# Optimization experiments

Hardware: AMD Instinct MI355X
Metric: run time of the kernel (lower is better)

The kernel has to match this reference:

```python
import jax, jax.numpy as jnp
import numpy as np

B, T, C, H = 2, 2048, 1024, 16
HD = C // H          # head_dim = 64
HALF = HD // 2       # rope half dim = 32
ROPE_BASE = 10000.0


def _build_sin_cos(seq_len, half_dim, base=ROPE_BASE):
    # mirrors build_sin_cos: angles[t, i] = t * base^(-2i / (2*half_dim))
    pos = jnp.arange(seq_len, dtype=jnp.float32)[:, None]                     # [T,1]
    inv_freq = 1.0 / (base ** (jnp.arange(0, half_dim * 2, 2, dtype=jnp.float32) / (half_dim * 2)))
    angles = pos * inv_freq                                                   # [T, half]
    return jnp.sin(angles), jnp.cos(angles)


def setup_inputs() -> dict:
    key = jax.random.key(0)
    k1, k2, k3 = jax.random.split(key, 3)
    x = jax.random.normal(k1, (B, T, C), dtype=jnp.float32)
    # nn.Linear weights (stored as [out,in] in torch; we keep [in,out] for x @ W)
    Wqkv = jax.random.normal(k2, (C, 3 * C), dtype=jnp.float32) * (C ** -0.5)
    Wproj = jax.random.normal(k3, (C, C), dtype=jnp.float32) * (C ** -0.5)
    rope_sin, rope_cos = _build_sin_cos(T, HALF)
    return {"x": x, "Wqkv": Wqkv, "Wproj": Wproj, "rope_sin": rope_sin, "rope_cos": rope_cos}


def reference(x, Wqkv, Wproj, rope_sin, rope_cos):
    Bb, Tt, Cc = x.shape
    Hh = H
    hd = Cc // Hh
    # fused QKV projection, then per-head split (matches view(B,T,H,3*hd).split)
    qkv = (x @ Wqkv).reshape(Bb, Tt, Hh, 3 * hd)
    q, k, v = jnp.split(qkv, 3, axis=-1)                                      # each [B,T,H,hd]
    # RoPE (single device path: local slice == full range)
    s = rope_sin[:Tt][None, :, None, :].astype(x.dtype)                       # [1,T,1,half]
    c = rope_cos[:Tt][None, :, None, :].astype(x.dtype)

    def rot(t):
        t1, t2 = jnp.split(t, 2, axis=-1)
        return jnp.concatenate([t1 * c - t2 * s, t1 * s + t2 * c], axis=-1)

    q = rot(q)
    k = rot(k)
    # causal scaled dot-product attention (flash_attn default scale = hd^-0.5)
    scale = jnp.asarray(hd, x.dtype) ** -0.5
    scores = jnp.einsum('bqhd,bkhd->bhqk', q, k) * scale                      # [B,H,T,T]
    causal = jnp.tril(jnp.ones((Tt, Tt), dtype=bool))
    scores = jnp.where(causal, scores, jnp.finfo(x.dtype).min)
    probs = jax.nn.softmax(scores, axis=-1)
    attn = jnp.einsum('bhqk,bkhd->bqhd', probs, v).reshape(Bb, Tt, Cc)
    return attn @ Wproj
```

## Files before the change

### kernel.cpp

```cpp
#include <hip/hip_runtime.h>

#define Bb 2
#define Tt 2048
#define Cc_ 1024
#define Hh 16
#define HDd 64

typedef __attribute__((ext_vector_type(8))) short bf16x8;
typedef __attribute__((ext_vector_type(4))) float f32x4;
typedef __attribute__((ext_vector_type(4))) unsigned short u16x4;
typedef __attribute__((ext_vector_type(2))) unsigned int u32x2;

__device__ __forceinline__ unsigned short f2bf(float f) {
  union { float f; unsigned int u; } v; v.f = f;
  unsigned int r = v.u + 0x7FFFu + ((v.u >> 16) & 1u);
  return (unsigned short)(r >> 16);
}
__device__ __forceinline__ float bf2f(unsigned short u) {
  union { unsigned int u; float f; } v; v.u = ((unsigned int)u) << 16;
  return v.f;
}
__device__ __forceinline__ unsigned int cvtpk(float lo, float hi) {
  unsigned int r;
  asm("v_cvt_pk_bf16_f32 %0, %1, %2" : "=v"(r) : "v"(lo), "v"(hi));
  return r;
}
__device__ __forceinline__ f32x4 mfma16(bf16x8 a, bf16x8 b, f32x4 c) {
  return __builtin_amdgcn_mfma_f32_16x16x32_bf16(a, b, c, 0, 0, 0);
}
__device__ __forceinline__ void gl_lds16(const void* g, void* l) {
  auto* gp = reinterpret_cast<const __attribute__((address_space(1))) unsigned int*>(
      reinterpret_cast<unsigned long long>(g));
  auto* lp = reinterpret_cast<__attribute__((address_space(3))) unsigned int*>(
      reinterpret_cast<unsigned long long>(l));
  __builtin_amdgcn_global_load_lds(gp, lp, 16, 0, 0);
}

__global__ __launch_bounds__(256) void k_prep(const float* __restrict__ x,
                                              const float* __restrict__ Wqkv,
                                              const float* __restrict__ Wproj,
                                              unsigned short* __restrict__ xb,
                                              unsigned short* __restrict__ wqkvt,
                                              unsigned short* __restrict__ wprot) {
  const int bid = blockIdx.x;
  const int tid = threadIdx.x;
  if (bid < 4096) {
    const int i = bid * 256 + tid;
    f32x4 v = ((const f32x4*)x)[i];
    u16x4 o;
    o[0] = f2bf(v[0]); o[1] = f2bf(v[1]); o[2] = f2bf(v[2]); o[3] = f2bf(v[3]);
    ((u16x4*)xb)[i] = o;
    return;
  }
  __shared__ float tile[32][33];
  const int tx = tid & 31, ty = tid >> 5;
  if (bid < 4096 + 3072) {
    const int tt = bid - 4096;
    const int n0 = (tt % 96) * 32, k0 = (tt / 96) * 32;
    const int region = n0 >> 10, nl = n0 & 1023;
    const int ob = (nl >> 6) * 192 + region * 64 + (nl & 63);
#pragma unroll
    for (int i = 0; i < 4; ++i)
      tile[ty + i * 8][tx] = Wqkv[(size_t)(k0 + ty + i * 8) * 3072 + ob + tx];
    __syncthreads();
#pragma unroll
    for (int i = 0; i < 4; ++i)
      wqkvt[(size_t)(n0 + ty + i * 8) * 1024 + k0 + tx] = f2bf(tile[tx][ty + i * 8]);
    return;
  }
  const int tt = bid - 7168;
  const int c0 = (tt & 31) * 32, r0 = (tt >> 5) * 32;
#pragma unroll
  for (int i = 0; i < 4; ++i)
    tile[ty + i * 8][tx] = Wproj[(size_t)(r0 + ty + i * 8) * 1024 + c0 + tx];
  __syncthreads();
#pragma unroll
  for (int i = 0; i < 4; ++i)
    wprot[(size_t)(c0 + ty + i * 8) * 1024 + r0 + tx] = f2bf(tile[tx][ty + i * 8]);
}

__global__ __launch_bounds__(256) void k_gemm_qkv(const unsigned short* __restrict__ A,
                                                  const unsigned short* __restrict__ Bt,
                                                  const float* __restrict__ rsin,
                                                  const float* __restrict__ rcos,
                                                  unsigned short* __restrict__ Qo,
                                                  unsigned short* __restrict__ Ko,
                                                  unsigned short* __restrict__ vtmp) {
  __shared__ unsigned short lA[128 * 64];
  __shared__ unsigned short lB[128 * 64];
  const int K = 1024;
  const int tid = threadIdx.x;
  const int lane = tid & 63, wid = tid >> 6;
  const int wr = wid >> 1, wc = wid & 1;
  const int bm = blockIdx.y * 128, bn = blockIdx.x * 128;
  const int l15 = lane & 15, l4 = lane >> 4;
  f32x4 acc[4][4];
#pragma unroll
  for (int i = 0; i < 4; ++i)
#pragma unroll
    for (int j = 0; j < 4; ++j) acc[i][j] = f32x4{0.f, 0.f, 0.f, 0.f};
  for (int t = 0; t < 16; ++t) {
    const int k0 = t << 6;
    __syncthreads();
#pragma unroll
    for (int i = 0; i < 4; ++i) {
      const int slot = i * 256 + tid;
      const int row = slot >> 3, g = slot & 7;
      const int gs = (g ^ (row & 7)) * 8;
      gl_lds16(A + (size_t)(bm + row) * K + k0 + gs, &lA[slot * 8]);
      gl_lds16(Bt + (size_t)(bn + row) * K + k0 + gs, &lB[slot * 8]);
    }
    __syncthreads();
#pragma unroll
    for (int ks = 0; ks < 2; ++ks) {
      bf16x8 af[4], bfr[4];
#pragma unroll
      for (int mf = 0; mf < 4; ++mf) {
        const int row = wr * 64 + mf * 16 + l15;
        const int g = ks * 4 + l4;
        af[mf] = *(const bf16x8*)&lA[row * 64 + ((g ^ (row & 7)) * 8)];
      }
#pragma unroll
      for (int nf = 0; nf < 4; ++nf) {
        const int row = wc * 64 + nf * 16 + l15;
        const int g = ks * 4 + l4;
        bfr[nf] = *(const bf16x8*)&lB[row * 64 + ((g ^ (row & 7)) * 8)];
      }
#pragma unroll
      for (int mf = 0; mf < 4; ++mf)
#pragma unroll
        for (int nf = 0; nf < 4; ++nf)
          acc[mf][nf] = mfma16(af[mf], bfr[nf], acc[mf][nf]);
    }
  }
  const int rb = bm + wr * 64 + l4 * 4;
  const int region = blockIdx.x >> 3;
  if (region < 2) {
    const int h = (blockIdx.x & 7) * 2 + wc;
    unsigned short* dst = (region == 0) ? Qo : Ko;
    const float qs = (region == 0) ? (0.125f * 1.44269504088896f) : 1.0f;
#pragma unroll
    for (int mf = 0; mf < 4; ++mf)
#pragma unroll
      for (int j = 0; j < 4; ++j) {
        const int trow = rb + mf * 16 + j;
        const int bi = trow >> 11, t = trow & 2047;
        const size_t rowb = ((size_t)(bi * Hh + h) * Tt + t) * 64;
#pragma unroll
        for (int nf = 0; nf < 2; ++nf) {
          const int d = nf * 16 + l15;
          const float sn = rsin[t * 32 + d], cs = rcos[t * 32 + d];
          const float a1 = acc[mf][nf][j], a2 = acc[mf][nf + 2][j];
          dst[rowb + d] = f2bf((a1 * cs - a2 * sn) * qs);
          dst[rowb + d + 32] = f2bf((a1 * sn + a2 * cs) * qs);
        }
      }
  } else {
    const int colb = (blockIdx.x & 7) * 128 + wc * 64;
#pragma unroll
    for (int mf = 0; mf < 4; ++mf)
#pragma unroll
      for (int nf = 0; nf < 4; ++nf)
#pragma unroll
        for (int j = 0; j < 4; ++j)
          vtmp[(size_t)(rb + mf * 16 + j) * 1024 + colb + nf * 16 + l15] =
              f2bf(acc[mf][nf][j]);
  }
}

__global__ __launch_bounds__(256) void k_vrep(const unsigned short* __restrict__ vtmp,
                                              unsigned short* __restrict__ Vt) {
  __shared__ unsigned short tile[32][72];
  const int bh = blockIdx.y;
  const int t0 = blockIdx.x * 32;
  const int tx = threadIdx.x, ty = threadIdx.y;
  const int b = bh >> 4, h = bh & 15;
#pragma unroll
  for (int i = 0; i < 4; ++i) {
    const int trow = ty + i * 8;
    const size_t r = (size_t)(b * Tt + t0 + trow) * 1024 + h * 64;
    tile[trow][tx] = vtmp[r + tx];
    tile[trow][tx + 32] = vtmp[r + 32 + tx];
  }
  __syncthreads();
#pragma unroll
  for (int i = 0; i < 8; ++i) {
    const int d = ty + i * 8;
    Vt[((size_t)bh * 64 + d) * Tt + t0 + tx] = tile[tx][d];
  }
}

__global__ __launch_bounds__(256, 4) void k_attn(const unsigned short* __restrict__ Q,
                                                 const unsigned short* __restrict__ Kt,
                                                 const unsigned short* __restrict__ Vt,
                                                 unsigned short* __restrict__ Aout) {
  __shared__ unsigned short lK[2 * 64 * 64];
  __shared__ unsigned short lV[2 * 64 * 64];
  __shared__ unsigned short lP[4 * 16 * 64];
  const int bid = blockIdx.x;
  const int xcd = bid & 7, ss = bid >> 3;
  const int cc = ss & 31, kk = ss >> 5;
  const int bh = xcd * 4 + kk;
  const int c2 = (cc + ((kk & 2) ? 16 : 0)) & 31;
  const int qt = (kk & 1) ? (31 - c2) : c2;
  const int b = bh >> 4, h = bh & 15;
  const int tid = threadIdx.x, lane = tid & 63, w = tid >> 6;
  const int l15 = lane & 15, l4 = lane >> 4;
  const int qb = qt * 64;
  const unsigned short* Kbh = Kt + (size_t)bh * Tt * 64;
  const unsigned short* Vbh = Vt + (size_t)bh * 64 * Tt;

  int fo[4][2];
#pragma unroll
  for (int a = 0; a < 4; ++a)
#pragma unroll
    for (int bb = 0; bb < 2; ++bb)
      fo[a][bb] = ((a * 16 + l15) * 64 + (((bb * 4 + l4) ^ (l15 & 7)) * 8)) * 2;
  int pwo[4];
#pragma unroll
  for (int nf = 0; nf < 4; ++nf)
    pwo[nf] = (l15 * 64 + (((nf * 2 + (l4 >> 1)) ^ (l15 & 7)) * 8) + (l4 & 1) * 4) * 2;
  char* const pB = (char*)lP + w * 2048;
  char* const kB0 = (char*)lK;
  char* const vB0 = (char*)lV;
  const int rA = tid >> 3;
  const int gsA = ((tid & 7) ^ (rA & 7)) * 8;
  const int kgA = rA * 64 + gsA;
  const int vgA = rA * 2048 + gsA;
  char* const ldKA = (char*)lK + tid * 16;
  char* const ldVA = (char*)lV + tid * 16;

#define STAGE(BUF, TT)                                                   \
  {                                                                      \
    const int kv_ = (TT) * 64;                                           \
    gl_lds16(Kbh + kv_ * 64 + kgA, ldKA + (BUF) * 8192);                 \
    gl_lds16(Kbh + kv_ * 64 + kgA + 32 * 64, ldKA + (BUF) * 8192 + 4096);\
    gl_lds16(Vbh + kv_ + vgA, ldVA + (BUF) * 8192);                      \
    gl_lds16(Vbh + kv_ + vgA + 32 * 2048, ldVA + (BUF) * 8192 + 4096);   \
  }

  const size_t qoff = ((size_t)bh * Tt + qb + w * 16 + l15) * 64 + l4 * 8;
  const bf16x8 qf0 = *(const bf16x8*)&Q[qoff];
  const bf16x8 qf1 = *(const bf16x8*)&Q[qoff + 32];
  f32x4 o[4];
#pragma unroll
  for (int i = 0; i < 4; ++i) o[i] = f32x4{0.f, 0.f, 0.f, 0.f};
  float mrun = -1e30f, lrun = 0.f;
  const int nt = qt + 1;

#define BODY(CUR, T, LASTT)                                                       \
  {                                                                               \
    if ((T) + 1 < nt) STAGE(CUR ^ 1, (T) + 1);                                    \
    f32x4 sv[4];                                                                  \
    _Pragma("unroll") for (int i = 0; i < 4; ++i) sv[i] = f32x4{0.f, 0.f, 0.f, 0.f}; \
    __builtin_amdgcn_s_setprio(1);                                                \
    _Pragma("unroll") for (int ks = 0; ks < 2; ++ks) {                            \
      const bf16x8 qa = ks ? qf1 : qf0;                                           \
      _Pragma("unroll") for (int nf = 0; nf < 4; ++nf) {                          \
        const bf16x8 kf = *(const bf16x8*)(kB0 + (CUR) * 8192 + fo[nf][ks]);      \
        sv[nf] = mfma16(kf, qa, sv[nf]);                                          \
      }                                                                           \
    }                                                                             \
    __builtin_amdgcn_s_setprio(0);                                                \
    if (LASTT) {                                                                  \
      _Pragma("unroll") for (int nf = 0; nf < 4; ++nf)                            \
        _Pragma("unroll") for (int j = 0; j < 4; ++j)                             \
          if (nf * 16 + l4 * 4 + j > w * 16 + l15) sv[nf][j] = -3e38f;            \
    }                                                                             \
    float mx = fmaxf(fmaxf(fmaxf(sv[0][0], sv[0][1]), fmaxf(sv[0][2], sv[0][3])), \
                     fmaxf(fmaxf(sv[1][0], sv[1][1]), fmaxf(sv[1][2], sv[1][3])));\
    mx = fmaxf(mx, fmaxf(fmaxf(fmaxf(sv[2][0], sv[2][1]), fmaxf(sv[2][2], sv[2][3])), \
                         fmaxf(fmaxf(sv[3][0], sv[3][1]), fmaxf(sv[3][2], sv[3][3])))); \
    if (!__all(mx - mrun <= 8.0f)) {                                              \
      mx = fmaxf(mx, __shfl_xor(mx, 16, 64));                                     \
      mx = fmaxf(mx, __shfl_xor(mx, 32, 64));                                     \
      const float mnew = fmaxf(mrun, mx);                                         \
      const float alpha = exp2f(mrun - mnew);                                     \
      lrun *= alpha;                                                              \
      float aj[4];                                                                \
      _Pragma("unroll") for (int j = 0; j < 4; ++j) aj[j] = __shfl(alpha, l4 * 4 + j, 64); \
      _Pragma("unroll") for (int df = 0; df < 4; ++df)                            \
        _Pragma("unroll") for (int j = 0; j < 4; ++j) o[df][j] *= aj[j];          \
      mrun = mnew;                                                                \
    }                                                                             \
    _Pragma("unroll") for (int nf = 0; nf < 4; ++nf) {                            \
      const float p0 = exp2f(sv[nf][0] - mrun), p1 = exp2f(sv[nf][1] - mrun);     \
      const float p2 = exp2f(sv[nf][2] - mrun), p3 = exp2f(sv[nf][3] - mrun);     \
      lrun += (p0 + p1) + (p2 + p3);                                              \
      u32x2 pk; pk[0] = cvtpk(p0, p1); pk[1] = cvtpk(p2, p3);                     \
      *(u32x2*)(pB + pwo[nf]) = pk;                                               \
    }                                                                             \
    __builtin_amdgcn_s_setprio(1);                                                \
    _Pragma("unroll") for (int kb = 0; kb < 2; ++kb) {                            \
      const bf16x8 pa = *(const bf16x8*)(pB + fo[0][kb]);                         \
      _Pragma("unroll") for (int df = 0; df < 4; ++df) {                          \
        const bf16x8 vb = *(const bf16x8*)(vB0 + (CUR) * 8192 + fo[df][kb]);      \
        o[df] = mfma16(pa, vb, o[df]);                                            \
      }                                                                           \
    }                                                                             \
    __builtin_amdgcn_s_setprio(0);                                                \
    if ((T) + 1 < nt) asm volatile("s_waitcnt vmcnt(0)" ::: "memory");            \
    __builtin_amdgcn_s_barrier();                                                 \
  }

  STAGE(0, 0);
  asm volatile("s_waitcnt vmcnt(0)" ::: "memory");
  __builtin_amdgcn_s_barrier();
  int t = 0;
  for (; t + 2 < nt; t += 2) {
    BODY(0, t, false);
    BODY(1, t + 1, false);
  }
  if (nt - t == 2) {
    BODY(0, t, false);
    BODY(1, t + 1, true);
  } else {
    BODY(0, t, true);
  }
#undef BODY
#undef STAGE

  lrun += __shfl_xor(lrun, 16, 64);
  lrun += __shfl_xor(lrun, 32, 64);
  const float rinv = 1.f / lrun;
  float lj[4];
#pragma unroll
  for (int j = 0; j < 4; ++j) lj[j] = __shfl(rinv, l4 * 4 + j, 64);
#pragma unroll
  for (int j = 0; j < 4; ++j) {
    const size_t rr = (size_t)(b * Tt + qb + w * 16 + l4 * 4 + j) * 1024 + h * 64 + l15;
#pragma unroll
    for (int df = 0; df < 4; ++df) Aout[rr + df * 16] = f2bf(o[df][j] * lj[j]);
  }
}

__global__ __launch_bounds__(256) void k_gemm2(const unsigned short* __restrict__ A,
                                               const unsigned short* __restrict__ Bt,
                                               float* __restrict__ Cout) {
  __shared__ unsigned short lA[2][128 * 64];
  __shared__ unsigned short lB[2][64 * 64];
  const int K = 1024, N = 1024;
  const int tid = threadIdx.x;
  const int lane = tid & 63, w = tid >> 6;
  const int bm = blockIdx.y * 128, bn = blockIdx.x * 64;
  const int l15 = lane & 15, l4 = lane >> 4;
  f32x4 acc[2][4];
#pragma unroll
  for (int i = 0; i < 2; ++i)
#pragma unroll
    for (int j = 0; j < 4; ++j) acc[i][j] = f32x4{0.f, 0.f, 0.f, 0.f};

#define STG(BUF, TT)                                                        \
  {                                                                         \
    const int k0 = (TT) << 6;                                               \
    _Pragma("unroll") for (int i = 0; i < 4; ++i) {                         \
      const int slot = i * 256 + tid;                                       \
      const int row = slot >> 3, g = slot & 7;                              \
      const int gs = (g ^ (row & 7)) * 8;                                   \
      gl_lds16(A + (size_t)(bm + row) * K + k0 + gs, &lA[BUF][slot * 8]);   \
    }                                                                       \
    _Pragma("unroll") for (int i = 0; i < 2; ++i) {                         \
      const int slot = i * 256 + tid;                                       \
      const int row = slot >> 3, g = slot & 7;                              \
      const int gs = (g ^ (row & 7)) * 8;                                   \
      gl_lds16(Bt + (size_t)(bn + row) * K + k0 + gs, &lB[BUF][slot * 8]);  \
    }                                                                       \
  }

  STG(0, 0);
  asm volatile("s_waitcnt vmcnt(0)" ::: "memory");
  __builtin_amdgcn_s_barrier();
  for (int t = 0; t < 16; ++t) {
    const int cur = t & 1;
    if (t + 1 < 16) STG(cur ^ 1, t + 1);
    __builtin_amdgcn_s_setprio(1);
#pragma unroll
    for (int ks = 0; ks < 2; ++ks) {
      bf16x8 af[2], bfr[4];
#pragma unroll
      for (int mf = 0; mf < 2; ++mf) {
        const int row = w * 32 + mf * 16 + l15;
        const int g = ks * 4 + l4;
        af[mf] = *(const bf16x8*)&lA[cur][row * 64 + ((g ^ (row & 7)) * 8)];
      }
#pragma unroll
      for (int nf = 0; nf < 4; ++nf) {
        const int row = nf * 16 + l15;
        const int g = ks * 4 + l4;
        bfr[nf] = *(const bf16x8*)&lB[cur][row * 64 + ((g ^ (row & 7)) * 8)];
      }
#pragma unroll
      for (int mf = 0; mf < 2; ++mf)
#pragma unroll
        for (int nf = 0; nf < 4; ++nf)
          acc[mf][nf] = mfma16(af[mf], bfr[nf], acc[mf][nf]);
    }
    __builtin_amdgcn_s_setprio(0);
    if (t + 1 < 16) asm volatile("s_waitcnt vmcnt(0)" ::: "memory");
    __builtin_amdgcn_s_barrier();
  }
#undef STG
  const int rb = bm + w * 32 + l4 * 4;
  const int cb = bn + l15;
#pragma unroll
  for (int mf = 0; mf < 2; ++mf)
#pragma unroll
    for (int nf = 0; nf < 4; ++nf)
#pragma unroll
      for (int j = 0; j < 4; ++j)
        Cout[(size_t)(rb + mf * 16 + j) * N + cb + nf * 16] = acc[mf][nf][j];
}

extern "C" void kernel_launch(void* const* d_in, const int* in_sizes, int n_in,
                              void* d_out, int out_size, void* d_ws, size_t ws_size,
                              hipStream_t stream) {
  const float* x = (const float*)d_in[0];
  const float* Wqkv = (const float*)d_in[1];
  const float* Wproj = (const float*)d_in[2];
  const float* rsin = (const float*)d_in[3];
  const float* rcos = (const float*)d_in[4];
  float* out = (float*)d_out;
  char* ws = (char*)d_ws;
  unsigned short* xb = (unsigned short*)(ws);
  unsigned short* wqkvt = (unsigned short*)(ws + (size_t)(8 << 20));
  unsigned short* wprot = (unsigned short*)(ws + (size_t)(14 << 20));
  unsigned short* vtmp = (unsigned short*)(ws + (size_t)(16 << 20));
  unsigned short* Q = (unsigned short*)(ws + (size_t)(40 << 20));
  unsigned short* K = (unsigned short*)(ws + (size_t)(48 << 20));
  unsigned short* Vt = (unsigned short*)(ws + (size_t)(56 << 20));
  unsigned short* attn = (unsigned short*)(ws + (size_t)(64 << 20));

  k_prep<<<8192, 256, 0, stream>>>(x, Wqkv, Wproj, xb, wqkvt, wprot);
  k_gemm_qkv<<<dim3(24, 32), 256, 0, stream>>>(xb, wqkvt, rsin, rcos, Q, K, vtmp);
  k_vrep<<<dim3(64, 32), dim3(32, 8), 0, stream>>>(vtmp, Vt);
  k_attn<<<1024, 256, 0, stream>>>(Q, K, Vt, attn);
  k_gemm2<<<dim3(16, 32), 256, 0, stream>>>(attn, wprot, out);
}
```

Before: 186.3 us.

## Double-buffer QKV GEMM loads and fuse V transpose into its epilogue

The QKV GEMM now double-buffers its LDS tiles. The next K-slice's global-to-LDS copy is issued before the MFMAs on the current slice, with one barrier per iteration and raised wave priority during compute. The V region's epilogue transposes the tile through LDS and writes Vt directly, which removes the separate k_vrep kernel and the vtmp round trip through global memory. In exchange, LDS use doubles to 64KB per block, which may lower occupancy, and the epilogue adds two extra barrier phases.

```diff
diff --git a/kernel.cpp b/kernel.cpp
--- a/kernel.cpp
+++ b/kernel.cpp
@@ -85,9 +85,9 @@
                                                   const float* __restrict__ rcos,
                                                   unsigned short* __restrict__ Qo,
                                                   unsigned short* __restrict__ Ko,
-                                                  unsigned short* __restrict__ vtmp) {
-  __shared__ unsigned short lA[128 * 64];
-  __shared__ unsigned short lB[128 * 64];
+                                                  unsigned short* __restrict__ Vt) {
+  __shared__ unsigned short lA[2][128 * 64];
+  __shared__ unsigned short lB[2][128 * 64];
   const int K = 1024;
   const int tid = threadIdx.x;
   const int lane = tid & 63, wid = tid >> 6;
@@ -99,18 +99,26 @@
   for (int i = 0; i < 4; ++i)
 #pragma unroll
     for (int j = 0; j < 4; ++j) acc[i][j] = f32x4{0.f, 0.f, 0.f, 0.f};
+
+#define STG(BUF, TT)                                                        \
+  {                                                                         \
+    const int k0 = (TT) << 6;                                               \
+    _Pragma("unroll") for (int i = 0; i < 4; ++i) {                         \
+      const int slot = i * 256 + tid;                                       \
+      const int row = slot >> 3, g = slot & 7;                              \
+      const int gs = (g ^ (row & 7)) * 8;                                   \
+      gl_lds16(A + (size_t)(bm + row) * K + k0 + gs, &lA[BUF][slot * 8]);   \
+      gl_lds16(Bt + (size_t)(bn + row) * K + k0 + gs, &lB[BUF][slot * 8]);  \
+    }                                                                       \
+  }
+
+  STG(0, 0);
+  asm volatile("s_waitcnt vmcnt(0)" ::: "memory");
+  __builtin_amdgcn_s_barrier();
   for (int t = 0; t < 16; ++t) {
-    const int k0 = t << 6;
-    __syncthreads();
-#pragma unroll
-    for (int i = 0; i < 4; ++i) {
-      const int slot = i * 256 + tid;
-      const int row = slot >> 3, g = slot & 7;
-      const int gs = (g ^ (row & 7)) * 8;
-      gl_lds16(A + (size_t)(bm + row) * K + k0 + gs, &lA[slot * 8]);
-      gl_lds16(Bt + (size_t)(bn + row) * K + k0 + gs, &lB[slot * 8]);
-    }
-    __syncthreads();
+    const int cur = t & 1;
+    if (t + 1 < 16) STG(cur ^ 1, t + 1);
+    __builtin_amdgcn_s_setprio(1);
 #pragma unroll
     for (int ks = 0; ks < 2; ++ks) {
       bf16x8 af[4], bfr[4];
@@ -118,13 +126,13 @@
       for (int mf = 0; mf < 4; ++mf) {
         const int row = wr * 64 + mf * 16 + l15;
         const int g = ks * 4 + l4;
-        af[mf] = *(const bf16x8*)&lA[row * 64 + ((g ^ (row & 7)) * 8)];
+        af[mf] = *(const bf16x8*)&lA[cur][row * 64 + ((g ^ (row & 7)) * 8)];
       }
 #pragma unroll
       for (int nf = 0; nf < 4; ++nf) {
         const int row = wc * 64 + nf * 16 + l15;
         const int g = ks * 4 + l4;
-        bfr[nf] = *(const bf16x8*)&lB[row * 64 + ((g ^ (row & 7)) * 8)];
+        bfr[nf] = *(const bf16x8*)&lB[cur][row * 64 + ((g ^ (row & 7)) * 8)];
       }
 #pragma unroll
       for (int mf = 0; mf < 4; ++mf)
@@ -132,7 +140,12 @@
         for (int nf = 0; nf < 4; ++nf)
           acc[mf][nf] = mfma16(af[mf], bfr[nf], acc[mf][nf]);
     }
-  }
+    __builtin_amdgcn_s_setprio(0);
+    if (t + 1 < 16) asm volatile("s_waitcnt vmcnt(0)" ::: "memory");
+    __builtin_amdgcn_s_barrier();
+  }
+#undef STG
+
   const int rb = bm + wr * 64 + l4 * 4;
   const int region = blockIdx.x >> 3;
   if (region < 2) {
@@ -156,37 +169,35 @@
         }
       }
   } else {
-    const int colb = (blockIdx.x & 7) * 128 + wc * 64;
-#pragma unroll
-    for (int mf = 0; mf < 4; ++mf)
-#pragma unroll
-      for (int nf = 0; nf < 4; ++nf)
-#pragma unroll
-        for (int j = 0; j < 4; ++j)
-          vtmp[(size_t)(rb + mf * 16 + j) * 1024 + colb + nf * 16 + l15] =
-              f2bf(acc[mf][nf][j]);
-  }
-}
-
-__global__ __launch_bounds__(256) void k_vrep(const unsigned short* __restrict__ vtmp,
-                                              unsigned short* __restrict__ Vt) {
-  __shared__ unsigned short tile[32][72];
-  const int bh = blockIdx.y;
-  const int t0 = blockIdx.x * 32;
-  const int tx = threadIdx.x, ty = threadIdx.y;
-  const int b = bh >> 4, h = bh & 15;
-#pragma unroll
-  for (int i = 0; i < 4; ++i) {
-    const int trow = ty + i * 8;
-    const size_t r = (size_t)(b * Tt + t0 + trow) * 1024 + h * 64;
-    tile[trow][tx] = vtmp[r + tx];
-    tile[trow][tx + 32] = vtmp[r + 32 + tx];
-  }
-  __syncthreads();
-#pragma unroll
-  for (int i = 0; i < 8; ++i) {
-    const int d = ty + i * 8;
-    Vt[((size_t)bh * 64 + d) * Tt + t0 + tx] = tile[tx][d];
+    unsigned short* tp = &lA[0][0];
+    const int h0 = (blockIdx.x & 7) * 2;
+    const int bi = bm >> 11, tbase = bm & 2047;
+    const int dd = tid >> 2, t0c = (tid & 3) * 32;
+#pragma unroll
+    for (int ph = 0; ph < 2; ++ph) {
+      if (wc == ph) {
+#pragma unroll
+        for (int mf = 0; mf < 4; ++mf)
+#pragma unroll
+          for (int nf = 0; nf < 4; ++nf)
+#pragma unroll
+            for (int j = 0; j < 4; ++j) {
+              const int tl = wr * 64 + mf * 16 + l4 * 4 + j;
+              const int dl = nf * 16 + l15;
+              tp[tl * 65 + dl] = f2bf(acc[mf][nf][j]);
+            }
+      }
+      __syncthreads();
+      const size_t ob = ((size_t)(bi * Hh + h0 + ph) * 64 + dd) * (size_t)Tt + tbase + t0c;
+#pragma unroll
+      for (int c = 0; c < 8; ++c) {
+        u16x4 v4;
+#pragma unroll
+        for (int e = 0; e < 4; ++e) v4[e] = tp[(t0c + c * 4 + e) * 65 + dd];
+        *(u16x4*)&Vt[ob + c * 4] = v4;
+      }
+      __syncthreads();
+    }
   }
 }
 
@@ -424,15 +435,13 @@
   unsigned short* xb = (unsigned short*)(ws);
   unsigned short* wqkvt = (unsigned short*)(ws + (size_t)(8 << 20));
   unsigned short* wprot = (unsigned short*)(ws + (size_t)(14 << 20));
-  unsigned short* vtmp = (unsigned short*)(ws + (size_t)(16 << 20));
   unsigned short* Q = (unsigned short*)(ws + (size_t)(40 << 20));
   unsigned short* K = (unsigned short*)(ws + (size_t)(48 << 20));
   unsigned short* Vt = (unsigned short*)(ws + (size_t)(56 << 20));
   unsigned short* attn = (unsigned short*)(ws + (size_t)(64 << 20));
 
   k_prep<<<8192, 256, 0, stream>>>(x, Wqkv, Wproj, xb, wqkvt, wprot);
-  k_gemm_qkv<<<dim3(24, 32), 256, 0, stream>>>(xb, wqkvt, rsin, rcos, Q, K, vtmp);
-  k_vrep<<<dim3(64, 32), dim3(32, 8), 0, stream>>>(vtmp, Vt);
+  k_gemm_qkv<<<dim3(24, 32), 256, 0, stream>>>(xb, wqkvt, rsin, rcos, Q, K, Vt);
   k_attn<<<1024, 256, 0, stream>>>(Q, K, Vt, attn);
   k_gemm2<<<dim3(16, 32), 256, 0, stream>>>(attn, wprot, out);
 }
```

Result: faster. 176.2 us (-5.4%).
